# Kernel optimization log

Measured on AMD Instinct MI355X. Metric: run time of the kernel, lower is better.

## Reference

```python
import jax, jax.numpy as jnp
import numpy as np

P, N, C, F = 3, 50000, 5, 68   # planes, nodes/plane, classes, in+node feats
E = 150000                     # edges/plane
EF, NF = 64, 64                # edge_features, node_features

def setup_inputs() -> dict:
    key = jax.random.key(0)
    ks = jax.random.split(key, 10)
    s = 0.1
    return {
        "x": jax.random.normal(ks[0], (P, N, C, F), jnp.float32),
        "edge_index": jax.random.randint(ks[1], (P, 2, E), 0, N, jnp.int64),
        "ew1": s * jax.random.normal(ks[2], (P, C, 2 * F, EF), jnp.float32),
        "eb1": s * jax.random.normal(ks[3], (P, C, EF), jnp.float32),
        "ew2": s * jax.random.normal(ks[4], (P, C, EF, 1), jnp.float32),
        "eb2": s * jax.random.normal(ks[5], (P, C, 1), jnp.float32),
        "nw1": s * jax.random.normal(ks[6], (P, C, 2 * F, NF), jnp.float32),
        "nb1": s * jax.random.normal(ks[7], (P, C, NF), jnp.float32),
        "nw2": s * jax.random.normal(ks[8], (P, C, NF, NF), jnp.float32),
        "nb2": s * jax.random.normal(ks[9], (P, C, NF), jnp.float32),
    }

def _plane(x, ei, ew1, eb1, ew2, eb2, nw1, nb1, nw2, nb2):
    # x: [N, C, F]; ei: [2, E]
    src, dst = ei[0], ei[1]
    x_j = x[src]                                   # [E, C, F] (source)
    x_i = x[dst]                                   # [E, C, F] (target)
    # edge net input is detached in the original module
    e_in = jax.lax.stop_gradient(jnp.concatenate([x_i, x_j], axis=-1))  # [E, C, 2F]
    h = jnp.tanh(jnp.einsum('ecf,cfo->eco', e_in, ew1) + eb1)           # [E, C, EF]
    logit = jnp.einsum('ecf,cfo->eco', h, ew2) + eb2                    # [E, C, 1]
    w = jax.nn.softmax(logit, axis=1)              # softmax over classes
    msg = w * x_j                                  # [E, C, F]
    aggr = jax.ops.segment_sum(msg, dst, num_segments=x.shape[0])       # [N, C, F]
    u_in = jnp.concatenate([x, aggr], axis=-1)     # [N, C, 2F]
    h2 = jnp.tanh(jnp.einsum('ncf,cfo->nco', u_in, nw1) + nb1)          # [N, C, NF]
    return jnp.tanh(jnp.einsum('ncf,cfo->nco', h2, nw2) + nb2)          # [N, C, NF]

def reference(x, edge_index, ew1, eb1, ew2, eb2, nw1, nb1, nw2, nb2):
    return jax.vmap(_plane)(x, edge_index, ew1, eb1, ew2, eb2, nw1, nb1, nw2, nb2)
```

## Files before the change

### kernel.cpp

```cpp
#include <hip/hip_runtime.h>
#include <hip/hip_fp16.h>
#include <math.h>

typedef unsigned int uint;
typedef __fp16 half2_t __attribute__((ext_vector_type(2)));
typedef _Float16 v8h __attribute__((ext_vector_type(8)));
typedef _Float16 v4h __attribute__((ext_vector_type(4)));
typedef float f32v4 __attribute__((ext_vector_type(4)));

#define NUM_P 3
#define NUM_N 50000
#define NUM_C 5
#define NUM_E 150000
#define CF 340
#define NB32 1563
#define TE 128
#define EB2 1172
#define TN 128
#define NB128 391
#define SROW 129
#define NSB 196
#define NSBP 50176
#define NST 44

#define AH_T   ((size_t)NUM_P * NUM_N * 170)
#define NW1_T  (NUM_P * NUM_C * 68 * 64)
#define NW2_T  (NUM_P * NUM_C * 32 * 64)
#define LG_T   ((size_t)NUM_P * NUM_C * NUM_E)
#define EWB_T  (NUM_P * NUM_C * 2 * 4 * 640)

__device__ __forceinline__ float fast_tanh(float x) {
    float a = __expf(2.0f * x);
    float t = __builtin_amdgcn_rcpf(a + 1.0f);
    return fmaf(-2.0f, t, 1.0f);
}

__device__ __forceinline__ float dot2f(half2_t a, half2_t b, float c) {
#if __has_builtin(__builtin_amdgcn_fdot2)
    return __builtin_amdgcn_fdot2(a, b, c, false);
#else
    return fmaf((float)a[0], (float)b[0], fmaf((float)a[1], (float)b[1], c));
#endif
}

__device__ __forceinline__ half2_t bc(uint u) { return __builtin_bit_cast(half2_t, u); }

__device__ __forceinline__ uint pk2(float a, float b) {
    half2_t h = __builtin_amdgcn_cvt_pkrtz(a, b);
    return __builtin_bit_cast(uint, h);
}

__device__ __forceinline__ v8h mk8(uint a, uint b, uint c, uint d) {
    uint4 u; u.x = a; u.y = b; u.z = c; u.w = d;
    return __builtin_bit_cast(v8h, u);
}

__global__ __launch_bounds__(256) void convert_x_kernel(
    const float4* __restrict__ x4, uint* __restrict__ xh,
    uint* __restrict__ xn, int write_xn)
{
    __shared__ uint lds[32 * 170];
    const int nb = blockIdx.x % NB32;
    const int p  = blockIdx.x / NB32;
    const int n0 = nb * 32;
    const int nvalid = (n0 + 32 <= NUM_N) ? 32 : (NUM_N - n0);
    const int t = threadIdx.x;

    const float4* src = x4 + ((size_t)p * NUM_N + n0) * 85;
    const int nf4 = nvalid * 85;
    #pragma unroll
    for (int it = 0; it < 11; ++it) {
        const int i = t + it * 256;
        if (i < nf4) {
            const float4 v = src[i];
            lds[2 * i]     = pk2(v.x, v.y);
            lds[2 * i + 1] = pk2(v.z, v.w);
        }
    }
    __syncthreads();

    const int nq = nvalid * 34;
    #pragma unroll 1
    for (int c = 0; c < NUM_C; ++c) {
        uint* dst = xh + ((size_t)(p * NUM_C + c) * NUM_N + n0) * 34;
        #pragma unroll
        for (int it = 0; it < 5; ++it) {
            const int i = t + it * 256;
            if (i < nq) {
                const int nl = i / 34, j = i - nl * 34;
                dst[i] = lds[nl * 170 + c * 34 + j];
            }
        }
    }

    if (write_xn) {
        uint* dstn = xn + ((size_t)p * NUM_N + n0) * 170;
        const int tot = nvalid * 170;
        #pragma unroll
        for (int it = 0; it < 22; ++it) {
            const int i = t + it * 256;
            if (i < tot) dstn[i] = lds[i];
        }
    }
}

__global__ __launch_bounds__(256) void pack_pairs_kernel(
    const float* __restrict__ in, uint* __restrict__ outp, int total)
{
    int i = blockIdx.x * 256 + threadIdx.x;
    if (i >= total) return;
    int t = i >> 6, o = i & 63;
    outp[i] = pk2(in[t * 128 + o], in[t * 128 + 64 + o]);
}

__global__ __launch_bounds__(256) void pack_edge_mfma_kernel(
    const float* __restrict__ ew1, uint* __restrict__ ewb)
{
    int i = blockIdx.x * 256 + threadIdx.x;
    if (i >= EWB_T) return;
    int g    = i / 5120;
    int rem  = i - g * 5120;
    int s    = rem / 2560;
    int rem2 = rem - s * 2560;
    int nt   = rem2 / 640;
    int u    = rem2 - nt * 640;

    int f0, o; bool valid;
    if (u < 512) {
        int kt = u >> 8, uu = u & 255;
        int lane = uu >> 2, pp = uu & 3;
        f0 = kt * 32 + (lane >> 4) * 8 + 2 * pp;
        o  = nt * 16 + (lane & 15);
        valid = true;
    } else {
        int uu = u - 512;
        int lane = uu >> 1, pp = uu & 1;
        f0 = 64 + (lane >> 4) * 4 + 2 * pp;
        o  = nt * 16 + (lane & 15);
        valid = ((lane >> 4) == 0);
    }
    float w0 = 0.f, w1 = 0.f;
    if (valid) {
        int f = s * 68 + f0;
        w0 = ew1[((size_t)g * 136 + f) * 64 + o];
        w1 = ew1[((size_t)g * 136 + f + 1) * 64 + o];
    }
    ewb[i] = pk2(w0, w1);
}

__global__ __launch_bounds__(128) void edge_mfma_kernel(
    const uint*  __restrict__ xh,
    const int*   __restrict__ ei,
    const uint*  __restrict__ ewb,
    const float* __restrict__ eb1,
    const float* __restrict__ ew2,
    const float* __restrict__ eb2,
    float*       __restrict__ logits)
{
    __shared__ uint smem[TE * 40];
    __shared__ int  ids[2][TE];

    const int g    = blockIdx.x / EB2;
    const int blk  = blockIdx.x - g * EB2;
    const int p    = g / NUM_C;
    const int e0   = blk * TE;
    const int t    = threadIdx.x;
    const int lane = t & 63;
    const int wv   = t >> 6;
    const int col  = lane & 15;
    const int G    = lane >> 4;

    {
        const int e  = e0 + t;
        const int ec = (e < NUM_E) ? e : (NUM_E - 1);
        ids[0][t] = ei[(p * 2 + 0) * NUM_E + ec];
        ids[1][t] = ei[(p * 2 + 1) * NUM_E + ec];
    }
    {
        const uint2 z = make_uint2(0u, 0u);
        *(uint2*)&smem[t * 40 + 34] = z;
        *(uint2*)&smem[t * 40 + 36] = z;
        *(uint2*)&smem[t * 40 + 38] = z;
    }

    const uint* slice = xh + (size_t)g * NUM_N * 34;

    float b1v[4], w2v[4];
    #pragma unroll
    for (int nt = 0; nt < 4; ++nt) {
        b1v[nt] = eb1[g * 64 + nt * 16 + col];
        w2v[nt] = ew2[g * 64 + nt * 16 + col];
    }

    f32v4 acc[4][4];
    #pragma unroll
    for (int m = 0; m < 4; ++m)
        #pragma unroll
        for (int nt = 0; nt < 4; ++nt) {
            f32v4 a = {b1v[nt], b1v[nt], b1v[nt], b1v[nt]};
            acc[m][nt] = a;
        }
    __syncthreads();

    #pragma unroll 1
    for (int side = 0; side < 2; ++side) {
        const int* idr = ids[1 - side];
        #pragma unroll
        for (int k = 0; k < 17; ++k) {
            const int i2 = t + TE * k;
            const int e  = i2 / 17, j2 = i2 - e * 17;
            const uint2 v = *(const uint2*)(slice + (size_t)idr[e] * 34 + 2 * j2);
            *(uint2*)&smem[e * 40 + 2 * j2] = v;
        }
        __syncthreads();

        const uint* wb = ewb + (size_t)((g * 2 + side) * 4) * 640;
        v8h B0[4], B1[4]; v4h B2[4];
        #pragma unroll
        for (int nt = 0; nt < 4; ++nt) {
            const uint* fb = wb + nt * 640;
            B0[nt] = __builtin_bit_cast(v8h, *(const uint4*)(fb + lane * 4));
            B1[nt] = __builtin_bit_cast(v8h, *(const uint4*)(fb + 256 + lane * 4));
            B2[nt] = __builtin_bit_cast(v4h, *(const uint2*)(fb + 512 + lane * 2));
        }

        #pragma unroll
        for (int m = 0; m < 4; ++m) {
            const uint* rp = &smem[(wv * 64 + m * 16 + col) * 40];
            const v8h A0 = __builtin_bit_cast(v8h, *(const uint4*)(rp + G * 4));
            const v8h A1 = __builtin_bit_cast(v8h, *(const uint4*)(rp + 16 + G * 4));
            const v4h A2 = __builtin_bit_cast(v4h, *(const uint2*)(rp + 32 + G * 2));
            #pragma unroll
            for (int nt = 0; nt < 4; ++nt) {
                acc[m][nt] = __builtin_amdgcn_mfma_f32_16x16x32_f16(A0, B0[nt], acc[m][nt], 0, 0, 0);
                acc[m][nt] = __builtin_amdgcn_mfma_f32_16x16x32_f16(A1, B1[nt], acc[m][nt], 0, 0, 0);
                acc[m][nt] = __builtin_amdgcn_mfma_f32_16x16x16f16(A2, B2[nt], acc[m][nt], 0, 0, 0);
            }
        }
        __syncthreads();
    }

    float* elds = (float*)smem;
    #pragma unroll
    for (int m = 0; m < 4; ++m) {
        #pragma unroll
        for (int r = 0; r < 4; ++r) {
            float part = 0.f;
            #pragma unroll
            for (int nt = 0; nt < 4; ++nt)
                part = fmaf(w2v[nt], fast_tanh(acc[m][nt][r]), part);
            elds[(wv * 64 + m * 16 + G * 4 + r) * 20 + col] = part;
        }
    }
    const float4 s0 = *(const float4*)&elds[t * 20 + 0];
    const float4 s1 = *(const float4*)&elds[t * 20 + 4];
    const float4 s2 = *(const float4*)&elds[t * 20 + 8];
    const float4 s3 = *(const float4*)&elds[t * 20 + 12];
    float lg = ((s0.x + s0.y) + (s0.z + s0.w)) + ((s1.x + s1.y) + (s1.z + s1.w))
             + ((s2.x + s2.y) + (s2.z + s2.w)) + ((s3.x + s3.y) + (s3.z + s3.w))
             + eb2[g];
    if (e0 + t < NUM_E) logits[(size_t)g * NUM_E + e0 + t] = lg;
}

__global__ __launch_bounds__(256) void softmax_kernel(
    const float* __restrict__ logits, float* __restrict__ wbuf)
{
    const int i = blockIdx.x * 256 + threadIdx.x;
    if (i >= NUM_P * NUM_E) return;
    const int p = i / NUM_E, e = i - p * NUM_E;
    const size_t base = (size_t)p * NUM_C * NUM_E + e;
    float l[NUM_C];
    #pragma unroll
    for (int c = 0; c < NUM_C; ++c) l[c] = logits[base + (size_t)c * NUM_E];
    float m = l[0];
    #pragma unroll
    for (int c = 1; c < NUM_C; ++c) m = fmaxf(m, l[c]);
    float s = 0.f;
    #pragma unroll
    for (int c = 0; c < NUM_C; ++c) { l[c] = __expf(l[c] - m); s += l[c]; }
    const float inv = __builtin_amdgcn_rcpf(s);
    #pragma unroll
    for (int c = 0; c < NUM_C; ++c) wbuf[base + (size_t)c * NUM_E] = l[c] * inv;
}

__global__ __launch_bounds__(256) void deg_kernel(
    const int* __restrict__ ei, int* __restrict__ deg)
{
    const int i = blockIdx.x * 256 + threadIdx.x;
    if (i >= NUM_P * NUM_E) return;
    const int p = i / NUM_E, e = i - p * NUM_E;
    const int dst = ei[(p * 2 + 1) * NUM_E + e];
    atomicAdd(&deg[p * NUM_N + dst], 1);
}

__global__ __launch_bounds__(256) void scan_block_kernel(
    const int* __restrict__ deg, int* __restrict__ intra, int* __restrict__ bsum)
{
    __shared__ int s[256];
    const int blk = blockIdx.x % NSB;
    const int p   = blockIdx.x / NSB;
    const int t   = threadIdx.x;
    const int n   = blk * 256 + t;
    const int d   = (n < NUM_N) ? deg[p * NUM_N + n] : 0;
    s[t] = d;
    __syncthreads();
    #pragma unroll
    for (int o = 1; o < 256; o <<= 1) {
        int v = (t >= o) ? s[t - o] : 0;
        __syncthreads();
        s[t] += v;
        __syncthreads();
    }
    if (n < NUM_N) intra[p * NSBP + n] = s[t] - d;
    if (t == 255) bsum[p * NSB + blk] = s[255];
}

__global__ __launch_bounds__(256) void scan_seg_kernel(
    const int* __restrict__ bsum, int* __restrict__ segoff)
{
    __shared__ int s[256];
    const int t = threadIdx.x;
    #pragma unroll 1
    for (int p = 0; p < NUM_P; ++p) {
        const int b = (t < NSB) ? bsum[p * NSB + t] : 0;
        s[t] = b;
        __syncthreads();
        #pragma unroll
        for (int o = 1; o < 256; o <<= 1) {
            int v = (t >= o) ? s[t - o] : 0;
            __syncthreads();
            s[t] += v;
            __syncthreads();
        }
        if (t < NSB) segoff[p * NSB + t] = s[t] - b;
        __syncthreads();
    }
}

__global__ __launch_bounds__(256) void fill_kernel(
    const int* __restrict__ ei, int* __restrict__ cursor,
    const int* __restrict__ intra, const int* __restrict__ segoff,
    int* __restrict__ csr_src, int* __restrict__ csr_eid)
{
    const int i = blockIdx.x * 256 + threadIdx.x;
    if (i >= NUM_P * NUM_E) return;
    const int p = i / NUM_E, e = i - p * NUM_E;
    const int src = ei[(p * 2 + 0) * NUM_E + e];
    const int dst = ei[(p * 2 + 1) * NUM_E + e];
    const int slot = atomicAdd(&cursor[p * NUM_N + dst], 1);
    const int pos  = segoff[p * NSB + (dst >> 8)] + intra[p * NSBP + dst] + slot;
    csr_src[(size_t)p * NUM_E + pos] = src;
    csr_eid[(size_t)p * NUM_E + pos] = e;
}

__global__ __launch_bounds__(256) void gather_kernel(
    const uint*  __restrict__ xn,
    const float* __restrict__ wbuf,
    const int*   __restrict__ csr_src,
    const int*   __restrict__ csr_eid,
    const int*   __restrict__ deg,
    const int*   __restrict__ intra,
    const int*   __restrict__ segoff,
    uint*        __restrict__ aggr)
{
    const int wslot = threadIdx.x >> 6;
    const int lane  = threadIdx.x & 63;
    const int gw = blockIdx.x * 4 + wslot;
    const int p  = gw / NUM_N;
    const int n  = gw - p * NUM_N;

    const int dg   = deg[p * NUM_N + n];
    const int off0 = segoff[p * NSB + (n >> 8)] + intra[p * NSBP + n];

    const int q1 = lane + 64, q2 = lane + 128;
    const int c0 = lane / 34;
    const int c1 = q1 / 34;
    const int c2 = q2 / 34;

    float a0 = 0.f, a1 = 0.f, a2 = 0.f, a3 = 0.f, a4 = 0.f, a5 = 0.f;

    #pragma unroll 1
    for (int d = 0; d < dg; ++d) {
        const int src = csr_src[(size_t)p * NUM_E + off0 + d];
        const int e   = csr_eid[(size_t)p * NUM_E + off0 + d];

        const float wa = wbuf[(size_t)(p * NUM_C + c0) * NUM_E + e];
        const float wb = wbuf[(size_t)(p * NUM_C + c1) * NUM_E + e];
        const float wc = (lane < 42) ? wbuf[(size_t)(p * NUM_C + c2) * NUM_E + e] : 0.f;

        const uint* row = xn + (size_t)(p * NUM_N + src) * 170;
        const uint u0 = row[lane];
        const uint u1 = row[q1];
        const uint u2 = (lane < 42) ? row[q2] : 0u;
        const half2_t h0 = bc(u0), h1 = bc(u1), h2 = bc(u2);
        a0 = fmaf(wa, (float)h0[0], a0);
        a1 = fmaf(wa, (float)h0[1], a1);
        a2 = fmaf(wb, (float)h1[0], a2);
        a3 = fmaf(wb, (float)h1[1], a3);
        a4 = fmaf(wc, (float)h2[0], a4);
        a5 = fmaf(wc, (float)h2[1], a5);
    }

    const int i0 = lane - c0 * 34;
    const int i1 = q1 - c1 * 34;
    const int i2 = q2 - c2 * 34;
    aggr[((size_t)(p * NUM_C + c0) * NUM_N + n) * 34 + i0] = pk2(a0, a1);
    aggr[((size_t)(p * NUM_C + c1) * NUM_N + n) * 34 + i1] = pk2(a2, a3);
    if (lane < 42)
        aggr[((size_t)(p * NUM_C + c2) * NUM_N + n) * 34 + i2] = pk2(a4, a5);
}

__global__ __launch_bounds__(256) void edge_scatter_kernel(
    const uint*  __restrict__ xh,
    const int*   __restrict__ ei,
    const float* __restrict__ logits,
    uint*        __restrict__ aggr)
{
    const int wslot = threadIdx.x >> 6;
    const int lane  = threadIdx.x & 63;
    const int gw    = blockIdx.x * 4 + wslot;
    const int p     = gw / NUM_E;
    const int e     = gw - p * NUM_E;

    const int src = ei[(p * 2 + 0) * NUM_E + e];
    const int dst = ei[(p * 2 + 1) * NUM_E + e];

    float l[NUM_C];
    #pragma unroll
    for (int c = 0; c < NUM_C; ++c)
        l[c] = logits[(size_t)(p * NUM_C + c) * NUM_E + e];
    float m = l[0];
    #pragma unroll
    for (int c = 1; c < NUM_C; ++c) m = fmaxf(m, l[c]);
    float s = 0.f;
    #pragma unroll
    for (int c = 0; c < NUM_C; ++c) { l[c] = __expf(l[c] - m); s += l[c]; }
    const float inv = __builtin_amdgcn_rcpf(s);
    const float wt0 = l[0] * inv, wt1 = l[1] * inv, wt2 = l[2] * inv,
                wt3 = l[3] * inv, wt4 = l[4] * inv;

    #pragma unroll
    for (int k = 0; k < 3; ++k) {
        const int q = lane + 64 * k;
        if (q < 170) {
            const int c   = q / 34;
            const int idx = q - c * 34;
            const float wv = (c == 0) ? wt0 : (c == 1) ? wt1 : (c == 2) ? wt2
                           : (c == 3) ? wt3 : wt4;
            const uint xv = xh[((size_t)(p * NUM_C + c) * NUM_N + src) * 34 + idx];
            half2_t mv = __builtin_amdgcn_cvt_pkrtz(wv, wv) * bc(xv);
            uint* ap = aggr + ((size_t)(p * NUM_C + c) * NUM_N + dst) * 34 + idx;
            unsafeAtomicAdd((__half2*)ap, __builtin_bit_cast(__half2, mv));
        }
    }
}

__global__ __launch_bounds__(256) void node_mfma_kernel(
    const uint*  __restrict__ xh,
    const uint*  __restrict__ aggr,
    const uint*  __restrict__ nwp,
    const uint*  __restrict__ n2p,
    const float* __restrict__ nb1,
    const float* __restrict__ nb2,
    float*       __restrict__ out)
{
    __shared__ uint smem[TN * NST];

    const int g    = blockIdx.x / NB128;
    const int blk  = blockIdx.x - g * NB128;
    const int p    = g / NUM_C;
    const int c    = g - p * NUM_C;
    const int n0   = blk * TN;
    const int t    = threadIdx.x;
    const int lane = t & 63;
    const int wv   = t >> 6;
    const int col  = lane & 15;
    const int G    = lane >> 4;
    const int nvalid = (n0 + TN <= NUM_N) ? TN : (NUM_N - n0);
    const int lim2   = nvalid * 17;

    if (t < TN) {
        const uint2 z = make_uint2(0u, 0u);
        *(uint2*)&smem[t * NST + 34] = z;
        *(uint2*)&smem[t * NST + 36] = z;
        *(uint2*)&smem[t * NST + 38] = z;
    }

    const uint* wgp = nwp + (size_t)g * 68 * 64;

    float b1v[4];
    #pragma unroll
    for (int nt = 0; nt < 4; ++nt) b1v[nt] = nb1[g * 64 + nt * 16 + col];

    f32v4 acc[2][4];
    #pragma unroll
    for (int mt = 0; mt < 2; ++mt)
        #pragma unroll
        for (int nt = 0; nt < 4; ++nt) {
            f32v4 a = {b1v[nt], b1v[nt], b1v[nt], b1v[nt]};
            acc[mt][nt] = a;
        }

    #pragma unroll 1
    for (int side = 0; side < 2; ++side) {
        const uint* srcp = (side == 0 ? xh : aggr) + ((size_t)g * NUM_N + n0) * 34;
        #pragma unroll
        for (int k = 0; k < 9; ++k) {
            const int i2 = t + 256 * k;
            if (i2 < TN * 17) {
                const int i2c = (i2 < lim2) ? i2 : (lim2 - 1);
                const uint2 v = *(const uint2*)(srcp + 2 * i2c);
                const int nl = i2 / 17, j2 = i2 - nl * 17;
                *(uint2*)&smem[nl * NST + 2 * j2] = v;
            }
        }
        __syncthreads();

        v8h B0[4], B1[4]; v4h B2[4];
        #pragma unroll
        for (int nt = 0; nt < 4; ++nt) {
            const int oc = nt * 16 + col;
            const int r0 = side * 34 + G * 4;
            B0[nt] = mk8(wgp[(r0 + 0) * 64 + oc], wgp[(r0 + 1) * 64 + oc],
                         wgp[(r0 + 2) * 64 + oc], wgp[(r0 + 3) * 64 + oc]);
            const int r1 = r0 + 16;
            B1[nt] = mk8(wgp[(r1 + 0) * 64 + oc], wgp[(r1 + 1) * 64 + oc],
                         wgp[(r1 + 2) * 64 + oc], wgp[(r1 + 3) * 64 + oc]);
            uint b2a = (G == 0) ? wgp[(side * 34 + 32) * 64 + oc] : 0u;
            uint b2b = (G == 0) ? wgp[(side * 34 + 33) * 64 + oc] : 0u;
            uint2 u2; u2.x = b2a; u2.y = b2b;
            B2[nt] = __builtin_bit_cast(v4h, u2);
        }

        #pragma unroll
        for (int mt = 0; mt < 2; ++mt) {
            const uint* rp = &smem[(wv * 32 + mt * 16 + col) * NST];
            const v8h A0 = __builtin_bit_cast(v8h, *(const uint4*)(rp + G * 4));
            const v8h A1 = __builtin_bit_cast(v8h, *(const uint4*)(rp + 16 + G * 4));
            const v4h A2 = __builtin_bit_cast(v4h, *(const uint2*)(rp + 32 + G * 2));
            #pragma unroll
            for (int nt = 0; nt < 4; ++nt) {
                acc[mt][nt] = __builtin_amdgcn_mfma_f32_16x16x32_f16(A0, B0[nt], acc[mt][nt], 0, 0, 0);
                acc[mt][nt] = __builtin_amdgcn_mfma_f32_16x16x32_f16(A1, B1[nt], acc[mt][nt], 0, 0, 0);
                acc[mt][nt] = __builtin_amdgcn_mfma_f32_16x16x16f16(A2, B2[nt], acc[mt][nt], 0, 0, 0);
            }
        }
        __syncthreads();
    }

    _Float16* hl = (_Float16*)smem;
    #pragma unroll
    for (int mt = 0; mt < 2; ++mt)
        #pragma unroll
        for (int nt = 0; nt < 4; ++nt)
            #pragma unroll
            for (int r = 0; r < 4; ++r)
                hl[(wv * 32 + mt * 16 + G * 4 + r) * 72 + nt * 16 + col] =
                    (_Float16)fast_tanh(acc[mt][nt][r]);

    const uint* w2p = n2p + (size_t)g * 32 * 64;
    float b2v[4];
    #pragma unroll
    for (int nt = 0; nt < 4; ++nt) b2v[nt] = nb2[g * 64 + nt * 16 + col];

    f32v4 acc2[2][4];
    #pragma unroll
    for (int mt = 0; mt < 2; ++mt)
        #pragma unroll
        for (int nt = 0; nt < 4; ++nt) {
            f32v4 a = {b2v[nt], b2v[nt], b2v[nt], b2v[nt]};
            acc2[mt][nt] = a;
        }

    v8h C0[4], C1[4];
    #pragma unroll
    for (int nt = 0; nt < 4; ++nt) {
        const int oc = nt * 16 + col;
        C0[nt] = mk8(w2p[(G * 4 + 0) * 64 + oc], w2p[(G * 4 + 1) * 64 + oc],
                     w2p[(G * 4 + 2) * 64 + oc], w2p[(G * 4 + 3) * 64 + oc]);
        C1[nt] = mk8(w2p[(16 + G * 4 + 0) * 64 + oc], w2p[(16 + G * 4 + 1) * 64 + oc],
                     w2p[(16 + G * 4 + 2) * 64 + oc], w2p[(16 + G * 4 + 3) * 64 + oc]);
    }

    #pragma unroll
    for (int mt = 0; mt < 2; ++mt) {
        const uint* rp = &smem[(wv * 32 + mt * 16 + col) * 36];
        const v8h A0 = __builtin_bit_cast(v8h, *(const uint4*)(rp + G * 4));
        const v8h A1 = __builtin_bit_cast(v8h, *(const uint4*)(rp + 16 + G * 4));
        #pragma unroll
        for (int nt = 0; nt < 4; ++nt) {
            acc2[mt][nt] = __builtin_amdgcn_mfma_f32_16x16x32_f16(A0, C0[nt], acc2[mt][nt], 0, 0, 0);
            acc2[mt][nt] = __builtin_amdgcn_mfma_f32_16x16x32_f16(A1, C1[nt], acc2[mt][nt], 0, 0, 0);
        }
    }
    __syncthreads();

    float* elds = (float*)smem;
    #pragma unroll
    for (int pass = 0; pass < 2; ++pass) {
        #pragma unroll
        for (int mt = 0; mt < 2; ++mt)
            #pragma unroll
            for (int r = 0; r < 4; ++r) {
                const int row = wv * 32 + mt * 16 + G * 4 + r;
                elds[row * NST + col]      = fast_tanh(acc2[mt][2 * pass][r]);
                elds[row * NST + 16 + col] = fast_tanh(acc2[mt][2 * pass + 1][r]);
            }
        const int row = wv * 32 + (lane >> 1);
        if (row < nvalid) {
            float* op = out + ((size_t)(p * NUM_N + n0 + row) * NUM_C + c) * 64
                      + pass * 32 + (lane & 1) * 16;
            const float* ep = &elds[row * NST + (lane & 1) * 16];
            #pragma unroll
            for (int q = 0; q < 4; ++q)
                *(float4*)(op + q * 4) = *(const float4*)(ep + q * 4);
        }
        if (pass == 0) __syncthreads();
    }
}

__device__ __forceinline__ void dot_side(const uint* __restrict__ xp,
                                         const uint* __restrict__ wp,
                                         float acc[64])
{
    uint2 cur = *(const uint2*)(xp);
    #pragma unroll 1
    for (int j = 0; j < 17; ++j) {
        const int jn = (j < 16) ? (j + 1) : 16;
        const uint2 nxt = *(const uint2*)(xp + jn * 2);
        const half2_t a0 = bc(cur.x);
        const half2_t a1 = bc(cur.y);
        const uint* w0 = wp + (2 * j) * 64;
        #pragma unroll
        for (int o = 0; o < 64; ++o)
            acc[o] = dot2f(a0, bc(w0[o]), acc[o]);
        const uint* w1 = w0 + 64;
        #pragma unroll
        for (int o = 0; o < 64; ++o)
            acc[o] = dot2f(a1, bc(w1[o]), acc[o]);
        cur = nxt;
    }
}

__global__ __launch_bounds__(128) void node_kernel(
    const float* __restrict__ x,
    const uint*  __restrict__ aggr,
    const uint*  __restrict__ nwp,
    const uint*  __restrict__ n2p,
    const float* __restrict__ nb1,
    const float* __restrict__ nb2,
    float*       __restrict__ out)
{
    __shared__ uint buf[34][SROW];

    const int g   = blockIdx.x / NB128;
    const int blk = blockIdx.x - g * NB128;
    const int p   = g / NUM_C;
    const int c   = g - p * NUM_C;
    const int n0  = blk * TN;
    const int t   = threadIdx.x;
    const int nvalid = (n0 + TN <= NUM_N) ? TN : (NUM_N - n0);
    const int lim2 = nvalid * 17;

    float acc[64];
    const float* b1 = nb1 + g * 64;
    #pragma unroll
    for (int o4 = 0; o4 < 64; o4 += 4) {
        const float4 bv = *(const float4*)(b1 + o4);
        acc[o4] = bv.x; acc[o4 + 1] = bv.y; acc[o4 + 2] = bv.z; acc[o4 + 3] = bv.w;
    }
    const uint* wg = nwp + (size_t)g * 68 * 64;

    #pragma unroll
    for (int k = 0; k < 34; ++k) {
        const int i  = t + TN * k;
        const int nl = i / 34, j = i - nl * 34;
        const int nn = (nl < nvalid) ? (n0 + nl) : n0;
        const float2 v = *(const float2*)(x + ((size_t)p * NUM_N + nn) * CF
                                          + c * 68 + 2 * j);
        buf[j][nl] = pk2(v.x, v.y);
    }
    __syncthreads();
    #pragma unroll 1
    for (int j = 0; j < 34; ++j) {
        const half2_t a = bc(buf[j][t]);
        const uint* w = wg + j * 64;
        #pragma unroll
        for (int o = 0; o < 64; ++o) acc[o] = dot2f(a, bc(w[o]), acc[o]);
    }
    __syncthreads();

    {
        const uint* srcp = aggr + ((size_t)g * NUM_N + n0) * 34;
        #pragma unroll
        for (int k = 0; k < 17; ++k) {
            const int i2  = t + TN * k;
            const int i2c = (i2 < lim2) ? i2 : (lim2 - 1);
            const uint2 v = *(const uint2*)(srcp + 2 * i2c);
            const int nl = i2 / 17, j2 = i2 - nl * 17;
            buf[2 * j2][nl]     = v.x;
            buf[2 * j2 + 1][nl] = v.y;
        }
    }
    __syncthreads();
    #pragma unroll 1
    for (int j = 0; j < 34; ++j) {
        const half2_t a = bc(buf[j][t]);
        const uint* w = wg + (34 + j) * 64;
        #pragma unroll
        for (int o = 0; o < 64; ++o) acc[o] = dot2f(a, bc(w[o]), acc[o]);
    }

    uint h2p[32];
    #pragma unroll
    for (int f2 = 0; f2 < 32; ++f2)
        h2p[f2] = pk2(fast_tanh(acc[2 * f2]), fast_tanh(acc[2 * f2 + 1]));

    const float* b2 = nb2 + g * 64;
    float acc2[64];
    #pragma unroll
    for (int o4 = 0; o4 < 64; o4 += 4) {
        const float4 bv = *(const float4*)(b2 + o4);
        acc2[o4] = bv.x; acc2[o4 + 1] = bv.y; acc2[o4 + 2] = bv.z; acc2[o4 + 3] = bv.w;
    }
    const uint* w2g = n2p + (size_t)g * 32 * 64;
    #pragma unroll
    for (int f2 = 0; f2 < 32; ++f2) {
        const half2_t hv = bc(h2p[f2]);
        const uint* wr = w2g + f2 * 64;
        #pragma unroll
        for (int o = 0; o < 64; ++o)
            acc2[o] = dot2f(hv, bc(wr[o]), acc2[o]);
    }

    if (t < nvalid) {
        float* op = out + ((size_t)(p * NUM_N + n0 + t) * NUM_C + c) * 64;
        #pragma unroll
        for (int o4 = 0; o4 < 64; o4 += 4) {
            float4 ov;
            ov.x = fast_tanh(acc2[o4 + 0]);
            ov.y = fast_tanh(acc2[o4 + 1]);
            ov.z = fast_tanh(acc2[o4 + 2]);
            ov.w = fast_tanh(acc2[o4 + 3]);
            *(float4*)(op + o4) = ov;
        }
    }
}

extern "C" void kernel_launch(void* const* d_in, const int* in_sizes, int n_in,
                              void* d_out, int out_size, void* d_ws, size_t ws_size,
                              hipStream_t stream)
{
    (void)in_sizes; (void)n_in; (void)out_size;

    const float* x   = (const float*)d_in[0];
    const int*   ei  = (const int*)  d_in[1];
    const float* ew1 = (const float*)d_in[2];
    const float* eb1 = (const float*)d_in[3];
    const float* ew2 = (const float*)d_in[4];
    const float* eb2 = (const float*)d_in[5];
    const float* nw1 = (const float*)d_in[6];
    const float* nb1 = (const float*)d_in[7];
    const float* nw2 = (const float*)d_in[8];
    const float* nb2 = (const float*)d_in[9];
    float*       out = (float*)d_out;

    uint* ws     = (uint*)d_ws;
    uint* aggr_h = ws;
    uint* nwp    = ws + AH_T;
    uint* n2p    = nwp + NW1_T;
    const size_t o_xh = AH_T + NW1_T + NW2_T;
    const bool fits = ws_size >= (o_xh + AH_T) * sizeof(uint);
    uint*  xh     = fits ? (ws + o_xh) : (uint*)d_out;
    uint*  xn     = (uint*)d_out;
    float* logits = (float*)((uint*)d_out + AH_T);
    uint*  ewb    = (uint*)d_out + AH_T + LG_T;

    int* ibase   = (int*)(ewb + EWB_T);
    int* deg     = ibase;
    int* cursor  = ibase + NUM_P * NUM_N;
    int* intra   = cursor + NUM_P * NUM_N;
    int* bsum    = intra + NUM_P * NSBP;
    int* segoff  = bsum + NUM_P * NSB;
    int* csr_src = segoff + NUM_P * NSB;
    int* csr_eid = csr_src + NUM_P * NUM_E;
    float* wbuf  = (float*)(csr_eid + NUM_P * NUM_E);

    convert_x_kernel<<<NUM_P * NB32, 256, 0, stream>>>(
        (const float4*)x, xh, xn, fits ? 1 : 0);
    pack_edge_mfma_kernel<<<(EWB_T + 255) / 256, 256, 0, stream>>>(ew1, ewb);
    pack_pairs_kernel<<<(NW1_T + 255) / 256, 256, 0, stream>>>(nw1, nwp, NW1_T);
    pack_pairs_kernel<<<(NW2_T + 255) / 256, 256, 0, stream>>>(nw2, n2p, NW2_T);

    edge_mfma_kernel<<<NUM_P * NUM_C * EB2, 128, 0, stream>>>(
        xh, ei, ewb, eb1, ew2, eb2, logits);

    if (fits) {
        (void)hipMemsetAsync(ibase, 0, (size_t)2 * NUM_P * NUM_N * sizeof(int), stream);
        const int egrid = (NUM_P * NUM_E + 255) / 256;
        softmax_kernel<<<egrid, 256, 0, stream>>>(logits, wbuf);
        deg_kernel<<<egrid, 256, 0, stream>>>(ei, deg);
        scan_block_kernel<<<NUM_P * NSB, 256, 0, stream>>>(deg, intra, bsum);
        scan_seg_kernel<<<1, 256, 0, stream>>>(bsum, segoff);
        fill_kernel<<<egrid, 256, 0, stream>>>(ei, cursor, intra, segoff,
                                               csr_src, csr_eid);
        gather_kernel<<<(NUM_P * NUM_N) / 4, 256, 0, stream>>>(
            xn, wbuf, csr_src, csr_eid, deg, intra, segoff, aggr_h);
        node_mfma_kernel<<<NUM_P * NUM_C * NB128, 256, 0, stream>>>(
            xh, aggr_h, nwp, n2p, nb1, nb2, out);
    } else {
        (void)hipMemsetAsync(aggr_h, 0, AH_T * sizeof(uint), stream);
        edge_scatter_kernel<<<(NUM_P * NUM_E) / 4, 256, 0, stream>>>(
            xh, ei, logits, aggr_h);
        node_kernel<<<NUM_P * NUM_C * NB128, 128, 0, stream>>>(
            x, aggr_h, nwp, n2p, nb1, nb2, out);
    }
}
```

Measured before the change: 599.5 us.

## Split edge MFMA tile across four waves and reduce logits with shuffles

The edge MLP kernel now runs with 256 threads (four waves) per 128-edge tile instead of two, so each wave owns 32 rows and holds half as many accumulators. The LDS row stride changes to NST (44), and the gather loop is reshaped for the larger block. The final per-edge logit reduction uses cross-lane shuffles and direct stores instead of an LDS transpose. The aim is more waves in flight and fewer registers per wave to hide gather latency. The cost is that each wave reloads the same B fragments and shuffle reductions replace a single vectorized LDS read.

Result: slower. 631.8 us (+5.4%).

```diff
diff --git a/kernel.cpp b/kernel.cpp
--- a/kernel.cpp
+++ b/kernel.cpp
@@ -148,7 +148,7 @@
     ewb[i] = pk2(w0, w1);
 }
 
-__global__ __launch_bounds__(128) void edge_mfma_kernel(
+__global__ __launch_bounds__(256) void edge_mfma_kernel(
     const uint*  __restrict__ xh,
     const int*   __restrict__ ei,
     const uint*  __restrict__ ewb,
@@ -157,7 +157,7 @@
     const float* __restrict__ eb2,
     float*       __restrict__ logits)
 {
-    __shared__ uint smem[TE * 40];
+    __shared__ uint smem[TE * NST];
     __shared__ int  ids[2][TE];
 
     const int g    = blockIdx.x / EB2;
@@ -170,18 +170,17 @@
     const int col  = lane & 15;
     const int G    = lane >> 4;
 
-    {
+    if (t < TE) {
         const int e  = e0 + t;
         const int ec = (e < NUM_E) ? e : (NUM_E - 1);
         ids[0][t] = ei[(p * 2 + 0) * NUM_E + ec];
         ids[1][t] = ei[(p * 2 + 1) * NUM_E + ec];
-    }
-    {
         const uint2 z = make_uint2(0u, 0u);
-        *(uint2*)&smem[t * 40 + 34] = z;
-        *(uint2*)&smem[t * 40 + 36] = z;
-        *(uint2*)&smem[t * 40 + 38] = z;
-    }
+        *(uint2*)&smem[t * NST + 34] = z;
+        *(uint2*)&smem[t * NST + 36] = z;
+        *(uint2*)&smem[t * NST + 38] = z;
+    }
+    __syncthreads();
 
     const uint* slice = xh + (size_t)g * NUM_N * 34;
 
@@ -192,25 +191,26 @@
         w2v[nt] = ew2[g * 64 + nt * 16 + col];
     }
 
-    f32v4 acc[4][4];
-    #pragma unroll
-    for (int m = 0; m < 4; ++m)
+    f32v4 acc[2][4];
+    #pragma unroll
+    for (int mt = 0; mt < 2; ++mt)
         #pragma unroll
         for (int nt = 0; nt < 4; ++nt) {
             f32v4 a = {b1v[nt], b1v[nt], b1v[nt], b1v[nt]};
-            acc[m][nt] = a;
-        }
-    __syncthreads();
+            acc[mt][nt] = a;
+        }
 
     #pragma unroll 1
     for (int side = 0; side < 2; ++side) {
         const int* idr = ids[1 - side];
         #pragma unroll
-        for (int k = 0; k < 17; ++k) {
-            const int i2 = t + TE * k;
-            const int e  = i2 / 17, j2 = i2 - e * 17;
-            const uint2 v = *(const uint2*)(slice + (size_t)idr[e] * 34 + 2 * j2);
-            *(uint2*)&smem[e * 40 + 2 * j2] = v;
+        for (int k = 0; k < 9; ++k) {
+            const int i2 = t + 256 * k;
+            if (i2 < TE * 17) {
+                const int e  = i2 / 17, j2 = i2 - e * 17;
+                const uint2 v = *(const uint2*)(slice + (size_t)idr[e] * 34 + 2 * j2);
+                *(uint2*)&smem[e * NST + 2 * j2] = v;
+            }
         }
         __syncthreads();
 
@@ -225,41 +225,40 @@
         }
 
         #pragma unroll
-        for (int m = 0; m < 4; ++m) {
-            const uint* rp = &smem[(wv * 64 + m * 16 + col) * 40];
+        for (int mt = 0; mt < 2; ++mt) {
+            const uint* rp = &smem[(wv * 32 + mt * 16 + col) * NST];
             const v8h A0 = __builtin_bit_cast(v8h, *(const uint4*)(rp + G * 4));
             const v8h A1 = __builtin_bit_cast(v8h, *(const uint4*)(rp + 16 + G * 4));
             const v4h A2 = __builtin_bit_cast(v4h, *(const uint2*)(rp + 32 + G * 2));
             #pragma unroll
             for (int nt = 0; nt < 4; ++nt) {
-                acc[m][nt] = __builtin_amdgcn_mfma_f32_16x16x32_f16(A0, B0[nt], acc[m][nt], 0, 0, 0);
-                acc[m][nt] = __builtin_amdgcn_mfma_f32_16x16x32_f16(A1, B1[nt], acc[m][nt], 0, 0, 0);
-                acc[m][nt] = __builtin_amdgcn_mfma_f32_16x16x16f16(A2, B2[nt], acc[m][nt], 0, 0, 0);
+                acc[mt][nt] = __builtin_amdgcn_mfma_f32_16x16x32_f16(A0, B0[nt], acc[mt][nt], 0, 0, 0);
+                acc[mt][nt] = __builtin_amdgcn_mfma_f32_16x16x32_f16(A1, B1[nt], acc[mt][nt], 0, 0, 0);
+                acc[mt][nt] = __builtin_amdgcn_mfma_f32_16x16x16f16(A2, B2[nt], acc[mt][nt], 0, 0, 0);
             }
         }
         __syncthreads();
     }
 
-    float* elds = (float*)smem;
-    #pragma unroll
-    for (int m = 0; m < 4; ++m) {
+    const float ebv = eb2[g];
+    #pragma unroll
+    for (int mt = 0; mt < 2; ++mt) {
         #pragma unroll
         for (int r = 0; r < 4; ++r) {
             float part = 0.f;
             #pragma unroll
             for (int nt = 0; nt < 4; ++nt)
-                part = fmaf(w2v[nt], fast_tanh(acc[m][nt][r]), part);
-            elds[(wv * 64 + m * 16 + G * 4 + r) * 20 + col] = part;
-        }
-    }
-    const float4 s0 = *(const float4*)&elds[t * 20 + 0];
-    const float4 s1 = *(const float4*)&elds[t * 20 + 4];
-    const float4 s2 = *(const float4*)&elds[t * 20 + 8];
-    const float4 s3 = *(const float4*)&elds[t * 20 + 12];
-    float lg = ((s0.x + s0.y) + (s0.z + s0.w)) + ((s1.x + s1.y) + (s1.z + s1.w))
-             + ((s2.x + s2.y) + (s2.z + s2.w)) + ((s3.x + s3.y) + (s3.z + s3.w))
-             + eb2[g];
-    if (e0 + t < NUM_E) logits[(size_t)g * NUM_E + e0 + t] = lg;
+                part = fmaf(w2v[nt], fast_tanh(acc[mt][nt][r]), part);
+            part += __shfl_xor(part, 1, 64);
+            part += __shfl_xor(part, 2, 64);
+            part += __shfl_xor(part, 4, 64);
+            part += __shfl_xor(part, 8, 64);
+            if (col == 0) {
+                const int e = e0 + wv * 32 + mt * 16 + G * 4 + r;
+                if (e < NUM_E) logits[(size_t)g * NUM_E + e] = part + ebv;
+            }
+        }
+    }
 }
 
 __global__ __launch_bounds__(256) void softmax_kernel(
@@ -792,7 +791,7 @@
     pack_pairs_kernel<<<(NW1_T + 255) / 256, 256, 0, stream>>>(nw1, nwp, NW1_T);
     pack_pairs_kernel<<<(NW2_T + 255) / 256, 256, 0, stream>>>(nw2, n2p, NW2_T);
 
-    edge_mfma_kernel<<<NUM_P * NUM_C * EB2, 128, 0, stream>>>(
+    edge_mfma_kernel<<<NUM_P * NUM_C * EB2, 256, 0, stream>>>(
         xh, ei, ewb, eb1, ew2, eb2, logits);
 
     if (fits) {
```

## Run edge MLP in CSR order so gather reads weights contiguously

Applied to the files above, without the earlier changes.

Builds the CSR before the edge MLP, which then processes edges in destination-sorted order using csr_src/csr_dst. The logits and softmax weights are therefore stored in CSR order, so the gather kernel reads them at consecutive positions instead of doing an indirect lookup through an edge-id array. This drops the csr_eid array and its loads, and sorted dst improves locality of x_i reads in the edge kernel. In exchange the edge kernel now depends on the CSR build having finished.

New measurement: 562.7 us, median of 2. 6.1% less time.

```diff
diff --git a/kernel.cpp b/kernel.cpp
--- a/kernel.cpp
+++ b/kernel.cpp
@@ -151,11 +151,14 @@
 __global__ __launch_bounds__(128) void edge_mfma_kernel(
     const uint*  __restrict__ xh,
     const int*   __restrict__ ei,
+    const int*   __restrict__ csr_src,
+    const int*   __restrict__ csr_dst,
     const uint*  __restrict__ ewb,
     const float* __restrict__ eb1,
     const float* __restrict__ ew2,
     const float* __restrict__ eb2,
-    float*       __restrict__ logits)
+    float*       __restrict__ logits,
+    int use_csr)
 {
     __shared__ uint smem[TE * 40];
     __shared__ int  ids[2][TE];
@@ -173,8 +176,13 @@
     {
         const int e  = e0 + t;
         const int ec = (e < NUM_E) ? e : (NUM_E - 1);
-        ids[0][t] = ei[(p * 2 + 0) * NUM_E + ec];
-        ids[1][t] = ei[(p * 2 + 1) * NUM_E + ec];
+        if (use_csr) {
+            ids[0][t] = csr_src[(size_t)p * NUM_E + ec];
+            ids[1][t] = csr_dst[(size_t)p * NUM_E + ec];
+        } else {
+            ids[0][t] = ei[(p * 2 + 0) * NUM_E + ec];
+            ids[1][t] = ei[(p * 2 + 1) * NUM_E + ec];
+        }
     }
     {
         const uint2 z = make_uint2(0u, 0u);
@@ -340,7 +348,7 @@
 __global__ __launch_bounds__(256) void fill_kernel(
     const int* __restrict__ ei, int* __restrict__ cursor,
     const int* __restrict__ intra, const int* __restrict__ segoff,
-    int* __restrict__ csr_src, int* __restrict__ csr_eid)
+    int* __restrict__ csr_src, int* __restrict__ csr_dst)
 {
     const int i = blockIdx.x * 256 + threadIdx.x;
     if (i >= NUM_P * NUM_E) return;
@@ -350,14 +358,13 @@
     const int slot = atomicAdd(&cursor[p * NUM_N + dst], 1);
     const int pos  = segoff[p * NSB + (dst >> 8)] + intra[p * NSBP + dst] + slot;
     csr_src[(size_t)p * NUM_E + pos] = src;
-    csr_eid[(size_t)p * NUM_E + pos] = e;
+    csr_dst[(size_t)p * NUM_E + pos] = dst;
 }
 
 __global__ __launch_bounds__(256) void gather_kernel(
     const uint*  __restrict__ xn,
     const float* __restrict__ wbuf,
     const int*   __restrict__ csr_src,
-    const int*   __restrict__ csr_eid,
     const int*   __restrict__ deg,
     const int*   __restrict__ intra,
     const int*   __restrict__ segoff,
@@ -381,12 +388,12 @@
 
     #pragma unroll 1
     for (int d = 0; d < dg; ++d) {
-        const int src = csr_src[(size_t)p * NUM_E + off0 + d];
-        const int e   = csr_eid[(size_t)p * NUM_E + off0 + d];
-
-        const float wa = wbuf[(size_t)(p * NUM_C + c0) * NUM_E + e];
-        const float wb = wbuf[(size_t)(p * NUM_C + c1) * NUM_E + e];
-        const float wc = (lane < 42) ? wbuf[(size_t)(p * NUM_C + c2) * NUM_E + e] : 0.f;
+        const int pos = off0 + d;
+        const int src = csr_src[(size_t)p * NUM_E + pos];
+
+        const float wa = wbuf[(size_t)(p * NUM_C + c0) * NUM_E + pos];
+        const float wb = wbuf[(size_t)(p * NUM_C + c1) * NUM_E + pos];
+        const float wc = (lane < 42) ? wbuf[(size_t)(p * NUM_C + c2) * NUM_E + pos] : 0.f;
 
         const uint* row = xn + (size_t)(p * NUM_N + src) * 170;
         const uint u0 = row[lane];
@@ -783,8 +790,8 @@
     int* bsum    = intra + NUM_P * NSBP;
     int* segoff  = bsum + NUM_P * NSB;
     int* csr_src = segoff + NUM_P * NSB;
-    int* csr_eid = csr_src + NUM_P * NUM_E;
-    float* wbuf  = (float*)(csr_eid + NUM_P * NUM_E);
+    int* csr_dst = csr_src + NUM_P * NUM_E;
+    float* wbuf  = (float*)(csr_dst + NUM_P * NUM_E);
 
     convert_x_kernel<<<NUM_P * NB32, 256, 0, stream>>>(
         (const float4*)x, xh, xn, fits ? 1 : 0);
@@ -792,23 +799,25 @@
     pack_pairs_kernel<<<(NW1_T + 255) / 256, 256, 0, stream>>>(nw1, nwp, NW1_T);
     pack_pairs_kernel<<<(NW2_T + 255) / 256, 256, 0, stream>>>(nw2, n2p, NW2_T);
 
-    edge_mfma_kernel<<<NUM_P * NUM_C * EB2, 128, 0, stream>>>(
-        xh, ei, ewb, eb1, ew2, eb2, logits);
-
     if (fits) {
         (void)hipMemsetAsync(ibase, 0, (size_t)2 * NUM_P * NUM_N * sizeof(int), stream);
         const int egrid = (NUM_P * NUM_E + 255) / 256;
-        softmax_kernel<<<egrid, 256, 0, stream>>>(logits, wbuf);
         deg_kernel<<<egrid, 256, 0, stream>>>(ei, deg);
         scan_block_kernel<<<NUM_P * NSB, 256, 0, stream>>>(deg, intra, bsum);
         scan_seg_kernel<<<1, 256, 0, stream>>>(bsum, segoff);
         fill_kernel<<<egrid, 256, 0, stream>>>(ei, cursor, intra, segoff,
-                                               csr_src, csr_eid);
+                                               csr_src, csr_dst);
+
+        edge_mfma_kernel<<<NUM_P * NUM_C * EB2, 128, 0, stream>>>(
+            xh, ei, csr_src, csr_dst, ewb, eb1, ew2, eb2, logits, 1);
+        softmax_kernel<<<egrid, 256, 0, stream>>>(logits, wbuf);
         gather_kernel<<<(NUM_P * NUM_N) / 4, 256, 0, stream>>>(
-            xn, wbuf, csr_src, csr_eid, deg, intra, segoff, aggr_h);
+            xn, wbuf, csr_src, deg, intra, segoff, aggr_h);
         node_mfma_kernel<<<NUM_P * NUM_C * NB128, 256, 0, stream>>>(
             xh, aggr_h, nwp, n2p, nb1, nb2, out);
     } else {
+        edge_mfma_kernel<<<NUM_P * NUM_C * EB2, 128, 0, stream>>>(
+            xh, ei, (const int*)ei, (const int*)ei, ewb, eb1, ew2, eb2, logits, 0);
         (void)hipMemsetAsync(aggr_h, 0, AH_T * sizeof(uint), stream);
         edge_scatter_kernel<<<(NUM_P * NUM_E) / 4, 256, 0, stream>>>(
             xh, ei, logits, aggr_h);
```
